# Performance work log

Hardware: AMD Instinct MI355X
Metric: run time of the kernel (lower is better)

Reference implementation:

```python
import jax, jax.numpy as jnp
import numpy as np

B = 16          # graphs per batch
N = 8192        # nodes per graph (equal-size graphs)
D = 256         # in_channels
RATIO = 0.5
K = int(np.ceil(RATIO * N))   # nodes kept per graph (PyG: ceil(ratio*N))
E = 2_097_152   # total edges (~avg_degree 16)


def setup_inputs() -> dict:
    key = jax.random.key(0)
    k1, k2, k3 = jax.random.split(key, 3)
    x = jax.random.normal(k1, (B * N, D), dtype=jnp.float32)
    # edges confined within each graph: local endpoint ids + graph offset
    local = jax.random.randint(k2, (2, E), 0, N)
    graph_of_edge = jnp.arange(E) // (E // B)            # [E]
    edge_index = local + graph_of_edge[None, :] * N      # [2, E] global node ids
    batch = jnp.repeat(jnp.arange(B), N)                 # [B*N]
    weight = jax.random.normal(k3, (D,), dtype=jnp.float32)  # TopKPooling score weight
    return {"x": x, "edge_index": edge_index, "batch": batch, "weight": weight}


def reference(x, edge_index, batch, weight):
    total = x.shape[0]
    # PyG TopKPooling: score = tanh((x . w) / ||w||)
    score = jnp.tanh((x @ weight) / jnp.linalg.norm(weight))   # [B*N]
    # per-graph top-k (equal-size graphs -> reshape)
    vals, idx = jax.lax.top_k(score.reshape(B, N), K)          # [B, K] each
    perm = (idx + jnp.arange(B)[:, None] * N).reshape(-1)      # [B*K] global kept ids
    x_out = x[perm] * vals.reshape(-1, 1)                      # gate features by score
    batch_out = batch[perm]
    # reindex: kept node i (in perm order) gets new id i, others -1 (PyG filter_adj)
    mapping = jnp.full((total,), -1, dtype=jnp.int32).at[perm].set(
        jnp.arange(B * K, dtype=jnp.int32))
    new_src = mapping[edge_index[0]]
    new_dst = mapping[edge_index[1]]
    kept = (new_src >= 0) & (new_dst >= 0)
    # fixed-shape padded edge_index: surviving edges reindexed, dropped edges = -1
    new_edge_index = jnp.where(kept[None, :], jnp.stack([new_src, new_dst]), -1)
    return x_out, new_edge_index, batch_out
```

## Files before the change

### kernel.cpp

```cpp
#include <hip/hip_runtime.h>

#define BGRAPH  16
#define NPG     8192
#define DIM     256
#define KKEEP   4096
#define TOTALN  (BGRAPH * NPG)
#define TOTKEEP (BGRAPH * KKEEP)
#define NEDGE   2097152
#define NBUCK   8192

using u16 = unsigned short;
using u32 = unsigned int;

__device__ __forceinline__ u32 desc_key(float f) {
  u32 b = __float_as_uint(f);
  u32 s = b ^ ((b & 0x80000000u) ? 0xFFFFFFFFu : 0x80000000u);
  return ~s;
}

__global__ __launch_bounds__(256) void k_score(const float* __restrict__ x,
                                               const float* __restrict__ w,
                                               float* __restrict__ score) {
  int gid  = blockIdx.x * 256 + threadIdx.x;
  int row  = gid >> 6;
  int lane = gid & 63;
  const float4 x4 = *reinterpret_cast<const float4*>(x + (size_t)row * DIM + lane * 4);
  const float4 w4 = *reinterpret_cast<const float4*>(w + lane * 4);
  double dot = (double)x4.x * w4.x + (double)x4.y * w4.y
             + (double)x4.z * w4.z + (double)x4.w * w4.w;
  double w2  = (double)w4.x * w4.x + (double)w4.y * w4.y
             + (double)w4.z * w4.z + (double)w4.w * w4.w;
  #pragma unroll
  for (int off = 32; off > 0; off >>= 1) {
    dot += __shfl_xor(dot, off, 64);
    w2  += __shfl_xor(w2,  off, 64);
  }
  if (lane == 0) score[row] = tanhf((float)(dot / sqrt(w2)));
}

__global__ __launch_bounds__(1024) void k_sort(const float* __restrict__ score,
                                               u32* __restrict__ skey,
                                               u16* __restrict__ sbkt,
                                               u32* __restrict__ bends) {
  __shared__ u32 hist[NBUCK];
  __shared__ u32 wsum[16];
  const int g    = blockIdx.x;
  const int tid  = threadIdx.x;
  const int wid  = tid >> 6;
  const int lane = tid & 63;
  const float* gs = score + (size_t)g * NPG;
  u32* skg = skey  + (size_t)g * NPG;
  u16* sbg = sbkt  + (size_t)g * NPG;
  u32* beg = bends + (size_t)g * NBUCK;

  #pragma unroll
  for (int i = 0; i < NBUCK / 1024; ++i) hist[tid + i * 1024] = 0;
  __syncthreads();

  u32 kd_[NPG / 1024];
  #pragma unroll
  for (int i = 0; i < NPG / 1024; ++i) {
    kd_[i] = desc_key(gs[tid + i * 1024]);
    atomicAdd(&hist[kd_[i] >> 19], 1u);
  }
  __syncthreads();

  u32 h[8], s = 0;
  #pragma unroll
  for (int j = 0; j < 8; ++j) { h[j] = hist[8 * tid + j]; s += h[j]; }
  u32 inc = s;
  #pragma unroll
  for (int off = 1; off < 64; off <<= 1) {
    u32 t = __shfl_up(inc, off, 64);
    if (lane >= off) inc += t;
  }
  if (lane == 63) wsum[wid] = inc;
  __syncthreads();
  if (tid < 16) {
    u32 v = wsum[tid], vi = v;
    #pragma unroll
    for (int off = 1; off < 16; off <<= 1) {
      u32 t = __shfl_up(vi, off, 64);
      if (tid >= off) vi += t;
    }
    wsum[tid] = vi - v;
  }
  __syncthreads();
  u32 run = inc - s + wsum[wid];
  #pragma unroll
  for (int j = 0; j < 8; ++j) { u32 hv = h[j]; hist[8 * tid + j] = run; run += hv; }
  __syncthreads();

  #pragma unroll
  for (int i = 0; i < NPG / 1024; ++i) {
    int idx = tid + i * 1024;
    u32 kd  = kd_[i];
    u32 b   = kd >> 19;
    u32 pos = atomicAdd(&hist[b], 1u);
    skg[pos] = (kd << 13) | (u32)idx;
    sbg[pos] = (u16)b;
  }
  __syncthreads();
  #pragma unroll
  for (int i = 0; i < NBUCK / 1024; ++i) {
    int b = tid + i * 1024;
    beg[b] = hist[b];
  }
}

__global__ __launch_bounds__(512) void k_count(const u32* __restrict__ skey,
                                               const u16* __restrict__ sbkt,
                                               const u32* __restrict__ bends,
                                               u16* __restrict__ map16) {
  const int g = blockIdx.x >> 4;
  const int p = (blockIdx.x & 15) * 512 + (int)threadIdx.x;
  const u32* skg = skey  + (size_t)g * NPG;
  const u32* beg = bends + (size_t)g * NBUCK;
  u32 key = skg[p];
  u32 b   = sbkt[(size_t)g * NPG + p];
  u32 start = b ? beg[b - 1] : 0;
  int idx = (int)(key & 0x1FFFu);
  u16* mp = map16 + ((size_t)g << 13);
  if (start >= KKEEP) { mp[idx] = (u16)0xFFFFu; return; }
  u32 end = beg[b];
  u32 cnt = 0, q = start;
  for (; q + 4 <= end; q += 4) {
    cnt += (skg[q]     < key) + (skg[q + 1] < key)
         + (skg[q + 2] < key) + (skg[q + 3] < key);
  }
  for (; q < end; ++q) cnt += (skg[q] < key);
  u32 rank = start + cnt;
  mp[idx] = (rank < KKEEP) ? (u16)rank : (u16)0xFFFFu;
}

__global__ __launch_bounds__(256) void k_gather(const float* __restrict__ x,
                                                const float* __restrict__ score,
                                                const u16* __restrict__ map16,
                                                float* __restrict__ x_out) {
  int gid  = blockIdx.x * 256 + threadIdx.x;
  int node = gid >> 6;
  int lane = gid & 63;
  u16 rk = map16[node];
  if (rk == 0xFFFFu) return;
  int nid = ((node >> 13) << 12) | (int)rk;
  float val = score[node];
  const float4 v = *reinterpret_cast<const float4*>(x + (size_t)node * DIM + lane * 4);
  float4 o;
  o.x = v.x * val; o.y = v.y * val; o.z = v.z * val; o.w = v.w * val;
  *reinterpret_cast<float4*>(x_out + (size_t)nid * DIM + lane * 4) = o;
}

__global__ __launch_bounds__(256) void k_edges(const int* __restrict__ ei,
                                               const u16* __restrict__ map16,
                                               float* __restrict__ e_out) {
  int e = blockIdx.x * 256 + threadIdx.x;
  int a = ei[e];
  int b = ei[NEDGE + e];
  u16 ra = map16[a];
  u16 rb = map16[b];
  bool kept = (ra != 0xFFFFu) && (rb != 0xFFFFu);
  e_out[e]         = kept ? (float)(((a >> 13) << 12) | (int)ra) : -1.0f;
  e_out[NEDGE + e] = kept ? (float)(((b >> 13) << 12) | (int)rb) : -1.0f;
}

__global__ __launch_bounds__(256) void k_batch(float* __restrict__ b_out) {
  int i = blockIdx.x * 256 + threadIdx.x;
  b_out[i] = (float)(i >> 12);
}

extern "C" void kernel_launch(void* const* d_in, const int* in_sizes, int n_in,
                              void* d_out, int out_size, void* d_ws, size_t ws_size,
                              hipStream_t stream) {
  const float* x  = nullptr;
  const int*   ei = nullptr;
  const float* w  = nullptr;
  for (int i = 0; i < n_in; ++i) {
    if      (in_sizes[i] == TOTALN * DIM) x  = (const float*)d_in[i];
    else if (in_sizes[i] == 2 * NEDGE)    ei = (const int*)d_in[i];
    else if (in_sizes[i] == DIM)          w  = (const float*)d_in[i];
  }
  (void)d_ws; (void)ws_size; (void)out_size;

  float* out   = (float*)d_out;
  float* x_out = out;
  float* e_out = out + (size_t)TOTKEEP * DIM;
  float* b_out = e_out + 2 * (size_t)NEDGE;

  float* score = e_out;
  u16*   map16 = (u16*)b_out;
  u32*   skey  = (u32*)x_out;
  u32*   bends = (u32*)(x_out + TOTALN);
  u16*   sbkt  = (u16*)(x_out + 2 * TOTALN);

  hipLaunchKernelGGL(k_score,  dim3(TOTALN / 4),    dim3(256),  0, stream, x, w, score);
  hipLaunchKernelGGL(k_sort,   dim3(BGRAPH),        dim3(1024), 0, stream, score, skey, sbkt, bends);
  hipLaunchKernelGGL(k_count,  dim3(BGRAPH * 16),   dim3(512),  0, stream, skey, sbkt, bends, map16);
  hipLaunchKernelGGL(k_gather, dim3(TOTALN / 4),    dim3(256),  0, stream, x, score, map16, x_out);
  hipLaunchKernelGGL(k_edges,  dim3(NEDGE / 256),   dim3(256),  0, stream, ei, map16, e_out);
  hipLaunchKernelGGL(k_batch,  dim3(TOTKEEP / 256), dim3(256),  0, stream, b_out);
}
```

Before: 94.20 us.

## Split per-graph bucket sort into grid-wide histogram, scan, and scatter kernels

The single 16-block sort kernel is replaced by three kernels: a grid-wide global-atomic histogram, a per-graph scan, and a grid-wide atomic scatter into buckets. The histogram is zeroed inside the score kernel. The aim is to stop running the sort on only 16 workgroups, which leaves most compute units idle. In exchange it adds two kernel launches and uses contended global atomics instead of LDS atomics. Scatter order inside a bucket becomes nondeterministic, but the count pass compares full keys, so ranks stay correct.

Measured after the change: 106.5 us. +13.1%, slower.

```diff
diff --git a/kernel.cpp b/kernel.cpp
--- a/kernel.cpp
+++ b/kernel.cpp
@@ -20,8 +20,10 @@
 
 __global__ __launch_bounds__(256) void k_score(const float* __restrict__ x,
                                                const float* __restrict__ w,
-                                               float* __restrict__ score) {
+                                               float* __restrict__ score,
+                                               u32* __restrict__ ghist) {
   int gid  = blockIdx.x * 256 + threadIdx.x;
+  if (gid < TOTALN) ghist[gid] = 0u;
   int row  = gid >> 6;
   int lane = gid & 63;
   const float4 x4 = *reinterpret_cast<const float4*>(x + (size_t)row * DIM + lane * 4);
@@ -38,36 +40,26 @@
   if (lane == 0) score[row] = tanhf((float)(dot / sqrt(w2)));
 }
 
-__global__ __launch_bounds__(1024) void k_sort(const float* __restrict__ score,
-                                               u32* __restrict__ skey,
-                                               u16* __restrict__ sbkt,
+__global__ __launch_bounds__(512) void k_hist(const float* __restrict__ score,
+                                              u32* __restrict__ ghist) {
+  int node = blockIdx.x * 512 + threadIdx.x;
+  u32 b = desc_key(score[node]) >> 19;
+  int g = node >> 13;
+  atomicAdd(&ghist[((u32)g << 13) | b], 1u);
+}
+
+__global__ __launch_bounds__(1024) void k_scan(u32* __restrict__ ghist,
                                                u32* __restrict__ bends) {
-  __shared__ u32 hist[NBUCK];
   __shared__ u32 wsum[16];
   const int g    = blockIdx.x;
   const int tid  = threadIdx.x;
   const int wid  = tid >> 6;
   const int lane = tid & 63;
-  const float* gs = score + (size_t)g * NPG;
-  u32* skg = skey  + (size_t)g * NPG;
-  u16* sbg = sbkt  + (size_t)g * NPG;
-  u32* beg = bends + (size_t)g * NBUCK;
-
-  #pragma unroll
-  for (int i = 0; i < NBUCK / 1024; ++i) hist[tid + i * 1024] = 0;
-  __syncthreads();
-
-  u32 kd_[NPG / 1024];
-  #pragma unroll
-  for (int i = 0; i < NPG / 1024; ++i) {
-    kd_[i] = desc_key(gs[tid + i * 1024]);
-    atomicAdd(&hist[kd_[i] >> 19], 1u);
-  }
-  __syncthreads();
-
+  u32* hg = ghist + ((size_t)g << 13);
+  u32* be = bends + ((size_t)g << 13);
   u32 h[8], s = 0;
   #pragma unroll
-  for (int j = 0; j < 8; ++j) { h[j] = hist[8 * tid + j]; s += h[j]; }
+  for (int j = 0; j < 8; ++j) { h[j] = hg[8 * tid + j]; s += h[j]; }
   u32 inc = s;
   #pragma unroll
   for (int off = 1; off < 64; off <<= 1) {
@@ -88,24 +80,26 @@
   __syncthreads();
   u32 run = inc - s + wsum[wid];
   #pragma unroll
-  for (int j = 0; j < 8; ++j) { u32 hv = h[j]; hist[8 * tid + j] = run; run += hv; }
-  __syncthreads();
+  for (int j = 0; j < 8; ++j) {
+    u32 hv = h[j];
+    hg[8 * tid + j] = run;
+    run += hv;
+    be[8 * tid + j] = run;
+  }
+}
 
-  #pragma unroll
-  for (int i = 0; i < NPG / 1024; ++i) {
-    int idx = tid + i * 1024;
-    u32 kd  = kd_[i];
-    u32 b   = kd >> 19;
-    u32 pos = atomicAdd(&hist[b], 1u);
-    skg[pos] = (kd << 13) | (u32)idx;
-    sbg[pos] = (u16)b;
-  }
-  __syncthreads();
-  #pragma unroll
-  for (int i = 0; i < NBUCK / 1024; ++i) {
-    int b = tid + i * 1024;
-    beg[b] = hist[b];
-  }
+__global__ __launch_bounds__(512) void k_scatter(const float* __restrict__ score,
+                                                 u32* __restrict__ ghist,
+                                                 u32* __restrict__ skey,
+                                                 u16* __restrict__ sbkt) {
+  int node = blockIdx.x * 512 + threadIdx.x;
+  int g    = node >> 13;
+  int idx  = node & (NPG - 1);
+  u32 kd   = desc_key(score[node]);
+  u32 b    = kd >> 19;
+  u32 pos  = atomicAdd(&ghist[((u32)g << 13) | b], 1u);
+  skey[((size_t)g << 13) | pos] = (kd << 13) | (u32)idx;
+  sbkt[((size_t)g << 13) | pos] = (u16)b;
 }
 
 __global__ __launch_bounds__(512) void k_count(const u32* __restrict__ skey,
@@ -114,10 +108,10 @@
                                                u16* __restrict__ map16) {
   const int g = blockIdx.x >> 4;
   const int p = (blockIdx.x & 15) * 512 + (int)threadIdx.x;
-  const u32* skg = skey  + (size_t)g * NPG;
-  const u32* beg = bends + (size_t)g * NBUCK;
+  const u32* skg = skey  + ((size_t)g << 13);
+  const u32* beg = bends + ((size_t)g << 13);
   u32 key = skg[p];
-  u32 b   = sbkt[(size_t)g * NPG + p];
+  u32 b   = sbkt[((size_t)g << 13) + p];
   u32 start = b ? beg[b - 1] : 0;
   int idx = (int)(key & 0x1FFFu);
   u16* mp = map16 + ((size_t)g << 13);
@@ -188,14 +182,17 @@
 
   float* score = e_out;
   u16*   map16 = (u16*)b_out;
-  u32*   skey  = (u32*)x_out;
+  u32*   ghist = (u32*)x_out;
   u32*   bends = (u32*)(x_out + TOTALN);
-  u16*   sbkt  = (u16*)(x_out + 2 * TOTALN);
+  u32*   skey  = (u32*)(x_out + 2 * TOTALN);
+  u16*   sbkt  = (u16*)(x_out + 3 * TOTALN);
 
-  hipLaunchKernelGGL(k_score,  dim3(TOTALN / 4),    dim3(256),  0, stream, x, w, score);
-  hipLaunchKernelGGL(k_sort,   dim3(BGRAPH),        dim3(1024), 0, stream, score, skey, sbkt, bends);
-  hipLaunchKernelGGL(k_count,  dim3(BGRAPH * 16),   dim3(512),  0, stream, skey, sbkt, bends, map16);
-  hipLaunchKernelGGL(k_gather, dim3(TOTALN / 4),    dim3(256),  0, stream, x, score, map16, x_out);
-  hipLaunchKernelGGL(k_edges,  dim3(NEDGE / 256),   dim3(256),  0, stream, ei, map16, e_out);
-  hipLaunchKernelGGL(k_batch,  dim3(TOTKEEP / 256), dim3(256),  0, stream, b_out);
+  hipLaunchKernelGGL(k_score,   dim3(TOTALN / 4),    dim3(256),  0, stream, x, w, score, ghist);
+  hipLaunchKernelGGL(k_hist,    dim3(TOTALN / 512),  dim3(512),  0, stream, score, ghist);
+  hipLaunchKernelGGL(k_scan,    dim3(BGRAPH),        dim3(1024), 0, stream, ghist, bends);
+  hipLaunchKernelGGL(k_scatter, dim3(TOTALN / 512),  dim3(512),  0, stream, score, ghist, skey, sbkt);
+  hipLaunchKernelGGL(k_count,   dim3(BGRAPH * 16),   dim3(512),  0, stream, skey, sbkt, bends, map16);
+  hipLaunchKernelGGL(k_gather,  dim3(TOTALN / 4),    dim3(256),  0, stream, x, score, map16, x_out);
+  hipLaunchKernelGGL(k_edges,   dim3(NEDGE / 256),   dim3(256),  0, stream, ei, map16, e_out);
+  hipLaunchKernelGGL(k_batch,   dim3(TOTKEEP / 256), dim3(256),  0, stream, b_out);
 }
```
